# Performance work log

Measured on AMD Instinct MI355X. Metric: run time of the kernel, lower is better.

The kernel has to match this reference:

```python
import jax, jax.numpy as jnp
import numpy as np

D = 1024
N = 8192

def setup_inputs() -> dict:
    key = jax.random.key(0)
    ks = jax.random.split(key, 9)
    s = 1.0 / np.sqrt(D)
    return {
        "queries": jax.random.normal(ks[0], (N, D), dtype=jnp.float32),
        "key": jax.random.normal(ks[1], (N, D), dtype=jnp.float32),
        "values": jax.random.normal(ks[2], (N, D), dtype=jnp.float32),
        "Wq": jax.random.normal(ks[3], (D, D), dtype=jnp.float32) * s,
        "bq": jnp.zeros((D,), dtype=jnp.float32),
        "Wk": jax.random.normal(ks[4], (D, D), dtype=jnp.float32) * s,
        "bk": jnp.zeros((D,), dtype=jnp.float32),
        "Wv": jax.random.normal(ks[5], (D, D), dtype=jnp.float32) * s,
        "bv": jnp.zeros((D,), dtype=jnp.float32),
    }

def reference(queries, key, values, Wq, bq, Wk, bk, Wv, bv):
    # Linear layers: x @ W^T + b (torch nn.Linear convention)
    q = queries @ Wq.T + bq          # [N, D]
    k = key @ Wk.T + bk              # [N, D]
    v = values @ Wv.T + bv           # [N, D]
    scale = 1.0 / jnp.sqrt(jnp.asarray(float(q.shape[-1]), dtype=q.dtype))
    scores = (q @ k.T) * scale       # [N, N]
    p = jax.nn.softmax(scores, axis=-1)  # legacy nn.Softmax() on 2D -> dim=1
    return p @ v                     # [N, D]
```

## Files before the change

kernel.cpp:

```cpp
#include <hip/hip_runtime.h>
#include <hip/hip_bf16.h>
#include <stdint.h>

#define NN 8192
#define DD 1024

typedef __attribute__((ext_vector_type(4))) float f32x4;
typedef __attribute__((ext_vector_type(8))) short bf16x8;
using bf16_t = __hip_bfloat16;

__device__ __forceinline__ void gload16(const void* g, void* l) {
  __builtin_amdgcn_global_load_lds(
      (const __attribute__((address_space(1))) void*)g,
      (__attribute__((address_space(3))) void*)l, 16, 0, 0);
}
__device__ __forceinline__ int imin(int a, int b) { return a < b ? a : b; }

__global__ __launch_bounds__(256) void cast_bf16_kernel(
    const float* __restrict__ in, bf16_t* __restrict__ out, int n8) {
  int i = blockIdx.x * 256 + threadIdx.x;
  if (i >= n8) return;
  const float4* p4 = (const float4*)in + (size_t)i * 2;
  float4 a = p4[0], b = p4[1];
  __align__(16) bf16_t tmp[8];
  tmp[0] = __float2bfloat16(a.x); tmp[1] = __float2bfloat16(a.y);
  tmp[2] = __float2bfloat16(a.z); tmp[3] = __float2bfloat16(a.w);
  tmp[4] = __float2bfloat16(b.x); tmp[5] = __float2bfloat16(b.y);
  tmp[6] = __float2bfloat16(b.z); tmp[7] = __float2bfloat16(b.w);
  *((uint4*)out + i) = *(const uint4*)tmp;
}

template<int MODE>
__global__ __launch_bounds__(256, 2)
void gemm_bt(const bf16_t* __restrict__ A, const bf16_t* __restrict__ B,
             const float* __restrict__ bias, void* __restrict__ Cout,
             int M, int Nc, int K, int ldc, float scale, int nbx) {
  __shared__ bf16_t As[128 * 32];
  __shared__ bf16_t Bs[128 * 32];
  const int t = threadIdx.x;
  const int nwg = gridDim.x;
  const int bid = (blockIdx.x & 7) * (nwg >> 3) + (blockIdx.x >> 3);
  const int bm = bid / nbx, bn = bid % nbx;
  const int lane = t & 63, wave = t >> 6;
  const int wr = wave >> 1, wc = wave & 1;

  const int c0 = t, c1 = t + 256;
  const bf16_t* ag0 = A + (size_t)(bm * 128 + (c0 >> 2)) * K + (c0 & 3) * 8;
  const bf16_t* ag1 = A + (size_t)(bm * 128 + (c1 >> 2)) * K + (c1 & 3) * 8;
  const bf16_t* bg0 = B + (size_t)(bn * 128 + (c0 >> 2)) * K + (c0 & 3) * 8;
  const bf16_t* bg1 = B + (size_t)(bn * 128 + (c1 >> 2)) * K + (c1 & 3) * 8;
  bf16_t* la0 = As + c0 * 8;
  bf16_t* la1 = As + c1 * 8;
  bf16_t* lb0 = Bs + c0 * 8;
  bf16_t* lb1 = Bs + c1 * 8;

  f32x4 acc[4][4] = {};
  const int fr = lane & 15;
  const int ko = (lane >> 4) * 8;

  for (int kt = 0; kt < K; kt += 32) {
    gload16(ag0 + kt, la0);
    gload16(ag1 + kt, la1);
    gload16(bg0 + kt, lb0);
    gload16(bg1 + kt, lb1);
    __syncthreads();
    bf16x8 af[4], bfv[4];
#pragma unroll
    for (int m = 0; m < 4; m++)
      af[m] = *(const bf16x8*)&As[(wr * 64 + m * 16 + fr) * 32 + ko];
#pragma unroll
    for (int n = 0; n < 4; n++)
      bfv[n] = *(const bf16x8*)&Bs[(wc * 64 + n * 16 + fr) * 32 + ko];
#pragma unroll
    for (int m = 0; m < 4; m++)
#pragma unroll
      for (int n = 0; n < 4; n++)
        acc[m][n] = __builtin_amdgcn_mfma_f32_16x16x32_bf16(af[m], bfv[n], acc[m][n], 0, 0, 0);
    __syncthreads();
  }

  const int rb = (lane >> 4) * 4;
#pragma unroll
  for (int m = 0; m < 4; m++) {
#pragma unroll
    for (int n = 0; n < 4; n++) {
      const int col = bn * 128 + wc * 64 + n * 16 + fr;
      const int row0 = bm * 128 + wr * 64 + m * 16 + rb;
      if (MODE == 0) {
        bf16_t* C = (bf16_t*)Cout;
        const float bv = bias[col];
#pragma unroll
        for (int j = 0; j < 4; j++)
          C[(size_t)(row0 + j) * ldc + col] = __float2bfloat16((acc[m][n][j] + bv) * scale);
      } else {
        bf16_t* C = (bf16_t*)Cout;
        const float bv = bias[col];
        __align__(8) bf16_t tmp[4];
#pragma unroll
        for (int j = 0; j < 4; j++)
          tmp[j] = __float2bfloat16((acc[m][n][j] + bv) * scale);
        *(ushort4*)&C[(size_t)col * ldc + row0] = *(const ushort4*)tmp;
      }
    }
  }
}

template<int MODE>
__global__ __launch_bounds__(512, 2)
void gemm256(const bf16_t* __restrict__ A, int lda,
             const bf16_t* __restrict__ B, int ldb,
             void* __restrict__ Cout, int ldc,
             float* __restrict__ aux, int ksplit, int nkt, int nbx, int Mrows) {
  __shared__ char smem_raw[131072];
  const int t = threadIdx.x;
  const int nwg = gridDim.x;
  const int bid = (blockIdx.x & 7) * (nwg >> 3) + (blockIdx.x >> 3);
  const int bm = bid / nbx, bn = bid % nbx;
  const int lane = t & 63, wave = t >> 6;
  const int wr = wave >> 2, wc = wave & 3;
  const int fr = lane & 15, hi = lane >> 4;
  const int k0 = blockIdx.y * ksplit;

  const int cswz = ((t & 7) ^ ((t >> 3) & 7)) * 8;
  uint32_t offA[2][2], offB[2][2];
#pragma unroll
  for (int h = 0; h < 2; h++)
#pragma unroll
    for (int l = 0; l < 2; l++) {
      const int r = h * 128 + l * 64 + (t >> 3);
      offA[h][l] = (uint32_t)((bm * 256 + r) * lda + k0 + cswz);
      offB[h][l] = (uint32_t)((bn * 256 + r) * ldb + k0 + cswz);
    }

  const int e = fr & 7;
  const int rowA = (wr * 128 + fr) * 128, rowB = (wc * 64 + fr) * 128;
  const int rdA_k0 = rowA + ((hi ^ e) << 4);
  const int rdA_k1 = rowA + (((hi + 4) ^ e) << 4);
  const int rdB_k0 = rowB + ((hi ^ e) << 4) + 32768;
  const int rdB_k1 = rowB + (((hi + 4) ^ e) << 4) + 32768;

  f32x4 acc[8][4] = {};
  bf16x8 af[4][2], bl[2][2], bh[2][2];

#define STA(buf, h, kt)                                                        \
  gload16(A + offA[h][0] + (size_t)(kt) * 64,                                  \
          smem_raw + (buf) * 65536 + (h) * 16384 + t * 16);                    \
  gload16(A + offA[h][1] + (size_t)(kt) * 64,                                  \
          smem_raw + (buf) * 65536 + (h) * 16384 + 8192 + t * 16);
#define STB(buf, h, kt)                                                        \
  gload16(B + offB[h][0] + (size_t)(kt) * 64,                                  \
          smem_raw + (buf) * 65536 + 32768 + (h) * 16384 + t * 16);            \
  gload16(B + offB[h][1] + (size_t)(kt) * 64,                                  \
          smem_raw + (buf) * 65536 + 32768 + (h) * 16384 + 8192 + t * 16);
#define RDA(buf, mf, ks)                                                       \
  (*(const bf16x8*)(smem_raw + (buf) * 65536 + ((ks) ? rdA_k1 : rdA_k0) +      \
                    (mf) * 2048))
#define RDB(buf, nf, ks)                                                       \
  (*(const bf16x8*)(smem_raw + (buf) * 65536 + ((ks) ? rdB_k1 : rdB_k0) +      \
                    (nf) * 2048))
#define MFMA8(BF, m0, n0)                                                      \
  _Pragma("unroll") for (int m = 0; m < 4; m++)                                \
  _Pragma("unroll") for (int n = 0; n < 2; n++)                                \
  _Pragma("unroll") for (int ks = 0; ks < 2; ks++)                             \
    acc[(m0) + m][(n0) + n] = __builtin_amdgcn_mfma_f32_16x16x32_bf16(         \
        af[m][ks], BF[n][ks], acc[(m0) + m][(n0) + n], 0, 0, 0);

  STB(0, 0, 0) STB(0, 1, 0) STA(0, 0, 0) STA(0, 1, 0)
  STB(1, 0, 1) STB(1, 1, 1)
  asm volatile("s_waitcnt vmcnt(4)" ::: "memory");
  __builtin_amdgcn_s_barrier();

  const int nit = nkt >> 1;
  for (int it = 0; it < nit; ++it) {
    const int T1 = 2 * it + 1;
    const int s2 = imin(2 * it + 2, nkt - 1);
    const int s3 = imin(2 * it + 3, nkt - 1);

#define TILEX(buf, S1, S2, S3, S4)                                             \
                                 \
    bl[0][0] = RDB(buf, 0, 0); bl[0][1] = RDB(buf, 0, 1);                      \
    bl[1][0] = RDB(buf, 1, 0); bl[1][1] = RDB(buf, 1, 1);                      \
    af[0][0] = RDA(buf, 0, 0); af[0][1] = RDA(buf, 0, 1);                      \
    af[1][0] = RDA(buf, 1, 0); af[1][1] = RDA(buf, 1, 1);                      \
    af[2][0] = RDA(buf, 2, 0); af[2][1] = RDA(buf, 2, 1);                      \
    af[3][0] = RDA(buf, 3, 0); af[3][1] = RDA(buf, 3, 1);                      \
    bh[0][0] = RDB(buf, 2, 0); bh[0][1] = RDB(buf, 2, 1);                      \
    bh[1][0] = RDB(buf, 3, 0); bh[1][1] = RDB(buf, 3, 1);                      \
    __builtin_amdgcn_s_setprio(1);                                             \
    MFMA8(bl, 0, 0)                                                            \
    MFMA8(bh, 0, 2)                                                            \
    __builtin_amdgcn_s_setprio(0);                                             \
                \
    __builtin_amdgcn_s_barrier();                                              \
    S1 S2 S3 S4                                                                \
    af[0][0] = RDA(buf, 4, 0); af[0][1] = RDA(buf, 4, 1);                      \
    af[1][0] = RDA(buf, 5, 0); af[1][1] = RDA(buf, 5, 1);                      \
    af[2][0] = RDA(buf, 6, 0); af[2][1] = RDA(buf, 6, 1);                      \
    af[3][0] = RDA(buf, 7, 0); af[3][1] = RDA(buf, 7, 1);                      \
    __builtin_amdgcn_s_setprio(1);                                             \
    MFMA8(bh, 4, 2)                                                            \
    MFMA8(bl, 4, 0)                                                            \
    __builtin_amdgcn_s_setprio(0);                                             \
    asm volatile("s_waitcnt vmcnt(4)" ::: "memory");                           \
    __builtin_amdgcn_s_barrier();

    TILEX(0, STA(1, 0, T1), STA(1, 1, T1), STB(0, 0, s2), STB(0, 1, s2))
    TILEX(1, STA(0, 0, s2), STA(0, 1, s2), STB(1, 0, s3), STB(1, 1, s3))
#undef TILEX
  }

  asm volatile("s_waitcnt vmcnt(0)" ::: "memory");
  __builtin_amdgcn_s_barrier();

  const int gr0 = bm * 256 + wr * 128 + hi * 4;
  const int gc0 = bn * 256 + wc * 64 + fr;

  if (MODE == 3) {
    float* rsum = (float*)smem_raw;
    if (t < 256) rsum[t] = 0.f;
    __syncthreads();
    bf16_t* C = (bf16_t*)Cout;
#pragma unroll
    for (int mf = 0; mf < 8; mf++) {
#pragma unroll
      for (int j = 0; j < 4; j++) {
        float rs = 0.f;
#pragma unroll
        for (int nf = 0; nf < 4; nf++) {
          float e2 = exp2f(acc[mf][nf][j] * 1.44269504088896f);
          bf16_t pb = __float2bfloat16(e2);
          C[(size_t)(gr0 + mf * 16 + j) * ldc + gc0 + nf * 16] = pb;
          rs += __bfloat162float(pb);
        }
        rs += __shfl_xor(rs, 1); rs += __shfl_xor(rs, 2);
        rs += __shfl_xor(rs, 4); rs += __shfl_xor(rs, 8);
        if (fr == 0) atomicAdd(&rsum[wr * 128 + mf * 16 + hi * 4 + j], rs);
      }
    }
    __syncthreads();
    if (t < 256) aux[(size_t)bn * Mrows + bm * 256 + t] = rsum[t];
  } else {
    float* C = blockIdx.y == 0 ? (float*)Cout : aux;
#pragma unroll
    for (int mf = 0; mf < 8; mf++)
#pragma unroll
      for (int nf = 0; nf < 4; nf++)
#pragma unroll
        for (int j = 0; j < 4; j++)
          C[(size_t)(gr0 + mf * 16 + j) * ldc + gc0 + nf * 16] = acc[mf][nf][j];
  }
#undef STA
#undef STB
#undef RDA
#undef RDB
#undef MFMA8
}

__global__ __launch_bounds__(256) void rowsum_inv_kernel(
    const float* __restrict__ partial, float* __restrict__ inv_l, int nb) {
  const int r = blockIdx.x * 256 + threadIdx.x;
  float s = 0.f;
  for (int b = 0; b < nb; b++) s += partial[(size_t)b * NN + r];
  inv_l[r] = 1.f / s;
}

__global__ __launch_bounds__(256) void combine_kernel(
    float* __restrict__ out, const float* __restrict__ o1,
    const float* __restrict__ inv_l) {
  const size_t i = (size_t)blockIdx.x * 256 + threadIdx.x;
  const float s = inv_l[(int)((i * 4) >> 10)];
  float4 a = ((const float4*)out)[i];
  const float4 b = ((const float4*)o1)[i];
  a.x = (a.x + b.x) * s; a.y = (a.y + b.y) * s;
  a.z = (a.z + b.z) * s; a.w = (a.w + b.w) * s;
  ((float4*)out)[i] = a;
}

extern "C" void kernel_launch(void* const* d_in, const int* in_sizes, int n_in,
                              void* d_out, int out_size, void* d_ws, size_t ws_size,
                              hipStream_t stream) {
  const float* queries = (const float*)d_in[0];
  const float* key_in  = (const float*)d_in[1];
  const float* values  = (const float*)d_in[2];
  const float* Wq = (const float*)d_in[3];
  const float* bq = (const float*)d_in[4];
  const float* Wk = (const float*)d_in[5];
  const float* bk = (const float*)d_in[6];
  const float* Wv = (const float*)d_in[7];
  const float* bv = (const float*)d_in[8];
  float* out = (float*)d_out;
  char* ws = (char*)d_ws;

  const size_t MB = 1024 * 1024;
  bf16_t* qb = (bf16_t*)(ws);
  bf16_t* kb = (bf16_t*)(ws + 16 * MB);
  bf16_t* vT = (bf16_t*)(ws + 32 * MB);
  bf16_t* P  = (bf16_t*)(ws + 48 * MB);
  float* partial = (float*)(ws + 176 * MB);
  float* inv_l   = (float*)(ws + 177 * MB);
  float* o1      = (float*)(ws + 178 * MB);
  bf16_t* xb = (bf16_t*)(ws + 48 * MB);
  bf16_t* wb = (bf16_t*)(ws + 64 * MB);

  const int nd8 = NN * DD / 8, dd8 = DD * DD / 8;

  cast_bf16_kernel<<<nd8 / 256, 256, 0, stream>>>(queries, xb, nd8);
  cast_bf16_kernel<<<dd8 / 256, 256, 0, stream>>>(Wq, wb, dd8);
  gemm_bt<0><<<(NN / 128) * (DD / 128), 256, 0, stream>>>(
      xb, wb, bq, qb, NN, DD, DD, DD, 0.03125f, DD / 128);
  cast_bf16_kernel<<<nd8 / 256, 256, 0, stream>>>(key_in, xb, nd8);
  cast_bf16_kernel<<<dd8 / 256, 256, 0, stream>>>(Wk, wb, dd8);
  gemm_bt<0><<<(NN / 128) * (DD / 128), 256, 0, stream>>>(
      xb, wb, bk, kb, NN, DD, DD, DD, 1.0f, DD / 128);
  cast_bf16_kernel<<<nd8 / 256, 256, 0, stream>>>(values, xb, nd8);
  cast_bf16_kernel<<<dd8 / 256, 256, 0, stream>>>(Wv, wb, dd8);
  gemm_bt<1><<<(NN / 128) * (DD / 128), 256, 0, stream>>>(
      xb, wb, bv, vT, NN, DD, DD, NN, 1.0f, DD / 128);

  gemm256<3><<<dim3((NN / 256) * (NN / 256)), 512, 0, stream>>>(
      qb, DD, kb, DD, P, NN, partial, 0, DD / 64, NN / 256, NN);
  rowsum_inv_kernel<<<NN / 256, 256, 0, stream>>>(partial, inv_l, NN / 256);
  gemm256<4><<<dim3((NN / 256) * (DD / 256), 2), 512, 0, stream>>>(
      P, NN, vT, NN, out, DD, o1, NN / 2, NN / 2 / 64, DD / 256, NN);
  combine_kernel<<<NN * DD / 4 / 256, 256, 0, stream>>>(out, o1, inv_l);
}
```

Baseline: 403.3 us.

## Switch GEMM inner loop from 16x16x32 to 32x32x16 bf16 MFMA tiles

Replaces the 16x16x32 MFMA fragments with 32x32x16 MFMA instructions. The per-wave 128x64 tile becomes a 4x2 grid of 32x32 accumulators, with LDS read offsets and epilogue row mapping rewritten to match. Larger MFMA tiles need fewer LDS fragment reads per FLOP and fewer instructions. The trade-off is a different read/compute interleave around the barrier and a new accumulator register layout, which could change register pressure and the amount of overlap.

```diff
diff --git a/kernel.cpp b/kernel.cpp
--- a/kernel.cpp
+++ b/kernel.cpp
@@ -6,6 +6,7 @@
 #define DD 1024
 
 typedef __attribute__((ext_vector_type(4))) float f32x4;
+typedef __attribute__((ext_vector_type(16))) float f32x16;
 typedef __attribute__((ext_vector_type(8))) short bf16x8;
 using bf16_t = __hip_bfloat16;
 
@@ -118,7 +119,7 @@
   const int bm = bid / nbx, bn = bid % nbx;
   const int lane = t & 63, wave = t >> 6;
   const int wr = wave >> 2, wc = wave & 3;
-  const int fr = lane & 15, hi = lane >> 4;
+  const int l31 = lane & 31, hi2 = lane >> 5;
   const int k0 = blockIdx.y * ksplit;
 
   const int cswz = ((t & 7) ^ ((t >> 3) & 7)) * 8;
@@ -132,15 +133,15 @@
       offB[h][l] = (uint32_t)((bn * 256 + r) * ldb + k0 + cswz);
     }
 
-  const int e = fr & 7;
-  const int rowA = (wr * 128 + fr) * 128, rowB = (wc * 64 + fr) * 128;
-  const int rdA_k0 = rowA + ((hi ^ e) << 4);
-  const int rdA_k1 = rowA + (((hi + 4) ^ e) << 4);
-  const int rdB_k0 = rowB + ((hi ^ e) << 4) + 32768;
-  const int rdB_k1 = rowB + (((hi + 4) ^ e) << 4) + 32768;
-
-  f32x4 acc[8][4] = {};
-  bf16x8 af[4][2], bl[2][2], bh[2][2];
+  const int e8 = l31 & 7;
+  const int rA0 = (wr * 128 + l31) * 128;
+  const int rB0 = 32768 + (wc * 64 + l31) * 128;
+  int ck[4];
+#pragma unroll
+  for (int ks = 0; ks < 4; ks++) ck[ks] = (((ks * 2 + hi2) ^ e8) << 4);
+
+  f32x16 acc[4][2] = {};
+  bf16x8 af[4], bfv[2][4];
 
 #define STA(buf, h, kt)                                                        \
   gload16(A + offA[h][0] + (size_t)(kt) * 64,                                  \
@@ -152,18 +153,19 @@
           smem_raw + (buf) * 65536 + 32768 + (h) * 16384 + t * 16);            \
   gload16(B + offB[h][1] + (size_t)(kt) * 64,                                  \
           smem_raw + (buf) * 65536 + 32768 + (h) * 16384 + 8192 + t * 16);
-#define RDA(buf, mf, ks)                                                       \
-  (*(const bf16x8*)(smem_raw + (buf) * 65536 + ((ks) ? rdA_k1 : rdA_k0) +      \
-                    (mf) * 2048))
-#define RDB(buf, nf, ks)                                                       \
-  (*(const bf16x8*)(smem_raw + (buf) * 65536 + ((ks) ? rdB_k1 : rdB_k0) +      \
-                    (nf) * 2048))
-#define MFMA8(BF, m0, n0)                                                      \
-  _Pragma("unroll") for (int m = 0; m < 4; m++)                                \
-  _Pragma("unroll") for (int n = 0; n < 2; n++)                                \
-  _Pragma("unroll") for (int ks = 0; ks < 2; ks++)                             \
-    acc[(m0) + m][(n0) + n] = __builtin_amdgcn_mfma_f32_16x16x32_bf16(         \
-        af[m][ks], BF[n][ks], acc[(m0) + m][(n0) + n], 0, 0, 0);
+#define RDA32(buf, mf, ks)                                                     \
+  (*(const bf16x8*)(smem_raw + (buf) * 65536 + rA0 + (mf) * 4096 + ck[ks]))
+#define RDB32(buf, nf, ks)                                                     \
+  (*(const bf16x8*)(smem_raw + (buf) * 65536 + rB0 + (nf) * 4096 + ck[ks]))
+#define MFMAK(buf, ks)                                                         \
+  af[0] = RDA32(buf, 0, ks); af[1] = RDA32(buf, 1, ks);                        \
+  af[2] = RDA32(buf, 2, ks); af[3] = RDA32(buf, 3, ks);                        \
+  __builtin_amdgcn_s_setprio(1);                                               \
+  _Pragma("unroll") for (int mf = 0; mf < 4; mf++)                             \
+  _Pragma("unroll") for (int nf = 0; nf < 2; nf++)                             \
+    acc[mf][nf] = __builtin_amdgcn_mfma_f32_32x32x16_bf16(                     \
+        af[mf], bfv[nf][ks], acc[mf][nf], 0, 0, 0);                            \
+  __builtin_amdgcn_s_setprio(0);
 
   STB(0, 0, 0) STB(0, 1, 0) STA(0, 0, 0) STA(0, 1, 0)
   STB(1, 0, 1) STB(1, 1, 1)
@@ -176,44 +178,31 @@
     const int s2 = imin(2 * it + 2, nkt - 1);
     const int s3 = imin(2 * it + 3, nkt - 1);
 
-#define TILEX(buf, S1, S2, S3, S4)                                             \
-                                 \
-    bl[0][0] = RDB(buf, 0, 0); bl[0][1] = RDB(buf, 0, 1);                      \
-    bl[1][0] = RDB(buf, 1, 0); bl[1][1] = RDB(buf, 1, 1);                      \
-    af[0][0] = RDA(buf, 0, 0); af[0][1] = RDA(buf, 0, 1);                      \
-    af[1][0] = RDA(buf, 1, 0); af[1][1] = RDA(buf, 1, 1);                      \
-    af[2][0] = RDA(buf, 2, 0); af[2][1] = RDA(buf, 2, 1);                      \
-    af[3][0] = RDA(buf, 3, 0); af[3][1] = RDA(buf, 3, 1);                      \
-    bh[0][0] = RDB(buf, 2, 0); bh[0][1] = RDB(buf, 2, 1);                      \
-    bh[1][0] = RDB(buf, 3, 0); bh[1][1] = RDB(buf, 3, 1);                      \
-    __builtin_amdgcn_s_setprio(1);                                             \
-    MFMA8(bl, 0, 0)                                                            \
-    MFMA8(bh, 0, 2)                                                            \
-    __builtin_amdgcn_s_setprio(0);                                             \
-                \
+#define TILE32(buf, S1, S2, S3, S4)                                            \
+                          \
+    bfv[0][0] = RDB32(buf, 0, 0); bfv[1][0] = RDB32(buf, 1, 0);                \
+    bfv[0][1] = RDB32(buf, 0, 1); bfv[1][1] = RDB32(buf, 1, 1);                \
+    bfv[0][2] = RDB32(buf, 0, 2); bfv[1][2] = RDB32(buf, 1, 2);                \
+    bfv[0][3] = RDB32(buf, 0, 3); bfv[1][3] = RDB32(buf, 1, 3);                \
+    MFMAK(buf, 0)                                                              \
+    \
     __builtin_amdgcn_s_barrier();                                              \
     S1 S2 S3 S4                                                                \
-    af[0][0] = RDA(buf, 4, 0); af[0][1] = RDA(buf, 4, 1);                      \
-    af[1][0] = RDA(buf, 5, 0); af[1][1] = RDA(buf, 5, 1);                      \
-    af[2][0] = RDA(buf, 6, 0); af[2][1] = RDA(buf, 6, 1);                      \
-    af[3][0] = RDA(buf, 7, 0); af[3][1] = RDA(buf, 7, 1);                      \
-    __builtin_amdgcn_s_setprio(1);                                             \
-    MFMA8(bh, 4, 2)                                                            \
-    MFMA8(bl, 4, 0)                                                            \
-    __builtin_amdgcn_s_setprio(0);                                             \
+    MFMAK(buf, 1)                                                              \
+    MFMAK(buf, 2)                                                              \
+    MFMAK(buf, 3)                                                              \
     asm volatile("s_waitcnt vmcnt(4)" ::: "memory");                           \
     __builtin_amdgcn_s_barrier();
 
-    TILEX(0, STA(1, 0, T1), STA(1, 1, T1), STB(0, 0, s2), STB(0, 1, s2))
-    TILEX(1, STA(0, 0, s2), STA(0, 1, s2), STB(1, 0, s3), STB(1, 1, s3))
-#undef TILEX
+    TILE32(0, STA(1, 0, T1), STA(1, 1, T1), STB(0, 0, s2), STB(0, 1, s2))
+    TILE32(1, STA(0, 0, s2), STA(0, 1, s2), STB(1, 0, s3), STB(1, 1, s3))
+#undef TILE32
   }
 
   asm volatile("s_waitcnt vmcnt(0)" ::: "memory");
   __builtin_amdgcn_s_barrier();
 
-  const int gr0 = bm * 256 + wr * 128 + hi * 4;
-  const int gc0 = bn * 256 + wc * 64 + fr;
+  const int gc0 = bn * 256 + wc * 64 + l31;
 
   if (MODE == 3) {
     float* rsum = (float*)smem_raw;
@@ -221,20 +210,23 @@
     __syncthreads();
     bf16_t* C = (bf16_t*)Cout;
 #pragma unroll
-    for (int mf = 0; mf < 8; mf++) {
-#pragma unroll
-      for (int j = 0; j < 4; j++) {
+    for (int mf = 0; mf < 4; mf++) {
+#pragma unroll
+      for (int reg = 0; reg < 16; reg++) {
+        const int lrow = wr * 128 + mf * 32 + (reg & 3) + 8 * (reg >> 2) + 4 * hi2;
+        const int grow = bm * 256 + lrow;
         float rs = 0.f;
 #pragma unroll
-        for (int nf = 0; nf < 4; nf++) {
-          float e2 = exp2f(acc[mf][nf][j] * 1.44269504088896f);
+        for (int nf = 0; nf < 2; nf++) {
+          float e2 = exp2f(acc[mf][nf][reg] * 1.44269504088896f);
           bf16_t pb = __float2bfloat16(e2);
-          C[(size_t)(gr0 + mf * 16 + j) * ldc + gc0 + nf * 16] = pb;
+          C[(size_t)grow * ldc + gc0 + nf * 32] = pb;
           rs += __bfloat162float(pb);
         }
         rs += __shfl_xor(rs, 1); rs += __shfl_xor(rs, 2);
         rs += __shfl_xor(rs, 4); rs += __shfl_xor(rs, 8);
-        if (fr == 0) atomicAdd(&rsum[wr * 128 + mf * 16 + hi * 4 + j], rs);
+        rs += __shfl_xor(rs, 16);
+        if (l31 == 0) atomicAdd(&rsum[lrow], rs);
       }
     }
     __syncthreads();
@@ -242,18 +234,20 @@
   } else {
     float* C = blockIdx.y == 0 ? (float*)Cout : aux;
 #pragma unroll
-    for (int mf = 0; mf < 8; mf++)
-#pragma unroll
-      for (int nf = 0; nf < 4; nf++)
-#pragma unroll
-        for (int j = 0; j < 4; j++)
-          C[(size_t)(gr0 + mf * 16 + j) * ldc + gc0 + nf * 16] = acc[mf][nf][j];
+    for (int mf = 0; mf < 4; mf++)
+#pragma unroll
+      for (int reg = 0; reg < 16; reg++) {
+        const int grow = bm * 256 + wr * 128 + mf * 32 + (reg & 3) + 8 * (reg >> 2) + 4 * hi2;
+#pragma unroll
+        for (int nf = 0; nf < 2; nf++)
+          C[(size_t)grow * ldc + gc0 + nf * 32] = acc[mf][nf][reg];
+      }
   }
 #undef STA
 #undef STB
-#undef RDA
-#undef RDB
-#undef MFMA8
+#undef RDA32
+#undef RDB32
+#undef MFMAK
 }
 
 __global__ __launch_bounds__(256) void rowsum_inv_kernel(
```

Measured after the change: 460.7 us. +14.2%, slower.

## Batch casts and projections into single launches, fold normalization into atomic split-K epilogue

Applied to the files above, without the earlier changes.

Six cast launches become one kernel over all inputs and weights, and the three projection GEMMs become one launch with blockIdx.y picking Q/K/V. The PV split-K GEMM now scales its partial results by the inverse row sum and atomically adds them into a zeroed output. This replaces the separate partial buffer and combine pass with a small zero pass. The aim is fewer launches, better occupancy for the projection GEMMs, and no extra full-size read and write in the combine. The cost is float atomics in the epilogue and a zeroing pass.

```diff
diff --git a/kernel.cpp b/kernel.cpp
--- a/kernel.cpp
+++ b/kernel.cpp
@@ -16,27 +16,51 @@
 }
 __device__ __forceinline__ int imin(int a, int b) { return a < b ? a : b; }
 
-__global__ __launch_bounds__(256) void cast_bf16_kernel(
-    const float* __restrict__ in, bf16_t* __restrict__ out, int n8) {
+__global__ __launch_bounds__(256) void cast6_kernel(
+    const float* __restrict__ i0, const float* __restrict__ i1,
+    const float* __restrict__ i2, const float* __restrict__ w0,
+    const float* __restrict__ w1, const float* __restrict__ w2,
+    bf16_t* __restrict__ out_x, bf16_t* __restrict__ out_w) {
+  const int nd8 = NN * DD / 8;
+  const int dd8 = DD * DD / 8;
   int i = blockIdx.x * 256 + threadIdx.x;
-  if (i >= n8) return;
-  const float4* p4 = (const float4*)in + (size_t)i * 2;
-  float4 a = p4[0], b = p4[1];
+  const float* src;
+  bf16_t* dst;
+  if (i < 3 * nd8) {
+    const int r = i >> 20, j = i & (nd8 - 1);
+    src = (r == 0 ? i0 : r == 1 ? i1 : i2) + (size_t)j * 8;
+    dst = out_x + (size_t)i * 8;
+  } else {
+    const int k = i - 3 * nd8;
+    const int r = k >> 17, j = k & (dd8 - 1);
+    src = (r == 0 ? w0 : r == 1 ? w1 : w2) + (size_t)j * 8;
+    dst = out_w + (size_t)k * 8;
+  }
+  const float4 a = ((const float4*)src)[0], b = ((const float4*)src)[1];
   __align__(16) bf16_t tmp[8];
   tmp[0] = __float2bfloat16(a.x); tmp[1] = __float2bfloat16(a.y);
   tmp[2] = __float2bfloat16(a.z); tmp[3] = __float2bfloat16(a.w);
   tmp[4] = __float2bfloat16(b.x); tmp[5] = __float2bfloat16(b.y);
   tmp[6] = __float2bfloat16(b.z); tmp[7] = __float2bfloat16(b.w);
-  *((uint4*)out + i) = *(const uint4*)tmp;
-}
-
-template<int MODE>
+  *(uint4*)dst = *(const uint4*)tmp;
+}
+
 __global__ __launch_bounds__(256, 2)
-void gemm_bt(const bf16_t* __restrict__ A, const bf16_t* __restrict__ B,
-             const float* __restrict__ bias, void* __restrict__ Cout,
-             int M, int Nc, int K, int ldc, float scale, int nbx) {
+void gemm_proj(const bf16_t* __restrict__ Abase, const bf16_t* __restrict__ Wbase,
+               const float* __restrict__ b0, const float* __restrict__ b1,
+               const float* __restrict__ b2, bf16_t* __restrict__ C0,
+               bf16_t* __restrict__ C1, bf16_t* __restrict__ C2) {
   __shared__ bf16_t As[128 * 32];
   __shared__ bf16_t Bs[128 * 32];
+  const int y = blockIdx.y;
+  const bf16_t* A = Abase + (size_t)y * NN * DD;
+  const bf16_t* B = Wbase + (size_t)y * DD * DD;
+  const float* bias = y == 0 ? b0 : y == 1 ? b1 : b2;
+  bf16_t* C = y == 0 ? C0 : y == 1 ? C1 : C2;
+  const float scale = y == 0 ? 0.03125f : 1.0f;
+  const int ldc = y == 2 ? NN : DD;
+  const int K = DD, nbx = DD / 128;
+
   const int t = threadIdx.x;
   const int nwg = gridDim.x;
   const int bid = (blockIdx.x & 7) * (nwg >> 3) + (blockIdx.x >> 3);
@@ -86,19 +110,16 @@
     for (int n = 0; n < 4; n++) {
       const int col = bn * 128 + wc * 64 + n * 16 + fr;
       const int row0 = bm * 128 + wr * 64 + m * 16 + rb;
-      if (MODE == 0) {
-        bf16_t* C = (bf16_t*)Cout;
-        const float bv = bias[col];
+      const float bv = bias[col];
+      if (y != 2) {
 #pragma unroll
         for (int j = 0; j < 4; j++)
           C[(size_t)(row0 + j) * ldc + col] = __float2bfloat16((acc[m][n][j] + bv) * scale);
       } else {
-        bf16_t* C = (bf16_t*)Cout;
-        const float bv = bias[col];
         __align__(8) bf16_t tmp[4];
 #pragma unroll
         for (int j = 0; j < 4; j++)
-          tmp[j] = __float2bfloat16((acc[m][n][j] + bv) * scale);
+          tmp[j] = __float2bfloat16(acc[m][n][j] + bv);
         *(ushort4*)&C[(size_t)col * ldc + row0] = *(const ushort4*)tmp;
       }
     }
@@ -240,14 +261,17 @@
     __syncthreads();
     if (t < 256) aux[(size_t)bn * Mrows + bm * 256 + t] = rsum[t];
   } else {
-    float* C = blockIdx.y == 0 ? (float*)Cout : aux;
+    float* C = (float*)Cout;
 #pragma unroll
     for (int mf = 0; mf < 8; mf++)
 #pragma unroll
-      for (int nf = 0; nf < 4; nf++)
-#pragma unroll
-        for (int j = 0; j < 4; j++)
-          C[(size_t)(gr0 + mf * 16 + j) * ldc + gc0 + nf * 16] = acc[mf][nf][j];
+      for (int j = 0; j < 4; j++) {
+        const int row = gr0 + mf * 16 + j;
+        const float s = aux[row];
+#pragma unroll
+        for (int nf = 0; nf < 4; nf++)
+          atomicAdd(&C[(size_t)row * ldc + gc0 + nf * 16], acc[mf][nf][j] * s);
+      }
   }
 #undef STA
 #undef STB
@@ -264,16 +288,8 @@
   inv_l[r] = 1.f / s;
 }
 
-__global__ __launch_bounds__(256) void combine_kernel(
-    float* __restrict__ out, const float* __restrict__ o1,
-    const float* __restrict__ inv_l) {
-  const size_t i = (size_t)blockIdx.x * 256 + threadIdx.x;
-  const float s = inv_l[(int)((i * 4) >> 10)];
-  float4 a = ((const float4*)out)[i];
-  const float4 b = ((const float4*)o1)[i];
-  a.x = (a.x + b.x) * s; a.y = (a.y + b.y) * s;
-  a.z = (a.z + b.z) * s; a.w = (a.w + b.w) * s;
-  ((float4*)out)[i] = a;
+__global__ __launch_bounds__(256) void zero_kernel(float4* __restrict__ p) {
+  p[(size_t)blockIdx.x * 256 + threadIdx.x] = make_float4(0.f, 0.f, 0.f, 0.f);
 }
 
 extern "C" void kernel_launch(void* const* d_in, const int* in_sizes, int n_in,
@@ -298,29 +314,19 @@
   bf16_t* P  = (bf16_t*)(ws + 48 * MB);
   float* partial = (float*)(ws + 176 * MB);
   float* inv_l   = (float*)(ws + 177 * MB);
-  float* o1      = (float*)(ws + 178 * MB);
-  bf16_t* xb = (bf16_t*)(ws + 48 * MB);
-  bf16_t* wb = (bf16_t*)(ws + 64 * MB);
+  bf16_t* x3 = (bf16_t*)(ws + 48 * MB);
+  bf16_t* w3 = (bf16_t*)(ws + 96 * MB);
 
   const int nd8 = NN * DD / 8, dd8 = DD * DD / 8;
 
-  cast_bf16_kernel<<<nd8 / 256, 256, 0, stream>>>(queries, xb, nd8);
-  cast_bf16_kernel<<<dd8 / 256, 256, 0, stream>>>(Wq, wb, dd8);
-  gemm_bt<0><<<(NN / 128) * (DD / 128), 256, 0, stream>>>(
-      xb, wb, bq, qb, NN, DD, DD, DD, 0.03125f, DD / 128);
-  cast_bf16_kernel<<<nd8 / 256, 256, 0, stream>>>(key_in, xb, nd8);
-  cast_bf16_kernel<<<dd8 / 256, 256, 0, stream>>>(Wk, wb, dd8);
-  gemm_bt<0><<<(NN / 128) * (DD / 128), 256, 0, stream>>>(
-      xb, wb, bk, kb, NN, DD, DD, DD, 1.0f, DD / 128);
-  cast_bf16_kernel<<<nd8 / 256, 256, 0, stream>>>(values, xb, nd8);
-  cast_bf16_kernel<<<dd8 / 256, 256, 0, stream>>>(Wv, wb, dd8);
-  gemm_bt<1><<<(NN / 128) * (DD / 128), 256, 0, stream>>>(
-      xb, wb, bv, vT, NN, DD, DD, NN, 1.0f, DD / 128);
-
+  cast6_kernel<<<(3 * nd8 + 3 * dd8) / 256, 256, 0, stream>>>(
+      queries, key_in, values, Wq, Wk, Wv, x3, w3);
+  gemm_proj<<<dim3((NN / 128) * (DD / 128), 3), 256, 0, stream>>>(
+      x3, w3, bq, bk, bv, qb, kb, vT);
   gemm256<3><<<dim3((NN / 256) * (NN / 256)), 512, 0, stream>>>(
       qb, DD, kb, DD, P, NN, partial, 0, DD / 64, NN / 256, NN);
   rowsum_inv_kernel<<<NN / 256, 256, 0, stream>>>(partial, inv_l, NN / 256);
+  zero_kernel<<<NN * DD / 4 / 256, 256, 0, stream>>>((float4*)out);
   gemm256<4><<<dim3((NN / 256) * (DD / 256), 2), 512, 0, stream>>>(
-      P, NN, vT, NN, out, DD, o1, NN / 2, NN / 2 / 64, DD / 256, NN);
-  combine_kernel<<<NN * DD / 4 / 256, 256, 0, stream>>>(out, o1, inv_l);
-}
+      P, NN, vT, NN, out, DD, inv_l, NN / 2, NN / 2 / 64, DD / 256, NN);
+}
```

New measurement: 401.4 us. No clear change (-0.5%).
